# Optimization experiments

Hardware: AMD Instinct MI355X
Metric: run time of the kernel (lower is better)

## Reference

```python
import jax, jax.numpy as jnp
import numpy as np

B, N, D_IN, D_OUT, HH, WW = 64, 512, 256, 32, 160, 160

def setup_inputs() -> dict:
    key = jax.random.key(0)
    k1, k2, k3, k4, k5 = jax.random.split(key, 5)
    return {
        "entity_embeddings": jax.random.normal(k1, (B, N, D_IN), dtype=jnp.float32),
        "weight": jax.random.normal(k2, (D_IN, D_OUT), dtype=jnp.float32) * (1.0 / np.sqrt(D_IN)),
        "bias": jnp.zeros((D_OUT,), dtype=jnp.float32),
        "entity_x": jax.random.randint(k3, (B, N), 0, WW, dtype=jnp.int32),
        "entity_y": jax.random.randint(k4, (B, N), 0, HH, dtype=jnp.int32),
        "entity_num": jax.random.randint(k5, (B,), 1, N, dtype=jnp.int32),
        "H": HH,
        "W": WW,
    }

def reference(entity_embeddings, weight, bias, entity_x, entity_y, entity_num, H, W):
    # fc_block: Linear + ReLU  -> [B, N, D_OUT]
    proj = jax.nn.relu(jnp.einsum('bni,io->bno', entity_embeddings, weight) + bias)
    # mask padded entities (sequence_mask from entity_num)
    mask = (jnp.arange(proj.shape[1])[None, :] < entity_num[:, None]).astype(proj.dtype)
    proj = proj * mask[:, :, None]
    # ScatterConnection ('add'): location = (y, x) -> flat index y*W + x
    flat_idx = entity_y.astype(jnp.int32) * W + entity_x.astype(jnp.int32)  # [B, N]
    b = proj.shape[0]
    out = jnp.zeros((b, H * W, proj.shape[2]), dtype=proj.dtype)
    out = out.at[jnp.arange(b)[:, None], flat_idx].add(proj)  # scatter-add
    # -> [B, D_OUT, H, W]
    scatter_map = out.reshape(b, H, W, proj.shape[2]).transpose(0, 3, 1, 2)
    return scatter_map
```

## Files before the change

kernel.cpp:

```cpp
#include <hip/hip_runtime.h>
#include <stdint.h>

constexpr int DIN  = 256;
constexpr int DOUT = 32;

typedef float f32x4  __attribute__((ext_vector_type(4)));
typedef short bf16x8 __attribute__((ext_vector_type(8)));


__device__ __forceinline__ uint16_t f2bf(float f, float& back) {
    uint32_t u = __builtin_bit_cast(uint32_t, f);
    uint32_t r = (u + 0x7fffu + ((u >> 16) & 1u)) >> 16;
    back = __builtin_bit_cast(float, r << 16);
    return (uint16_t)r;
}

__global__ __launch_bounds__(256)
void k_prep(const float* __restrict__ weight,
            uint16_t* __restrict__ wfh, uint16_t* __restrict__ wfl)
{
    const int id = blockIdx.x * 256 + threadIdx.x;
    const int t    = id >> 7;
    const int h    = (id >> 6) & 1;
    const int lane = id & 63;
    const int kb   = t * 32 + (lane >> 4) * 8;
    const int col  = h * 16 + (lane & 15);
    const int off  = ((t * 2 + h) * 64 + lane) * 8;
    #pragma unroll
    for (int j = 0; j < 8; ++j) {
        float w = weight[(size_t)(kb + j) * DOUT + col];
        float back; uint16_t hi = f2bf(w, back);
        float resid = w - back;
        float b2;  uint16_t lo = f2bf(resid, b2);
        wfh[off + j] = hi;
        wfl[off + j] = lo;
    }
}

__global__ __launch_bounds__(256)
void k_gemm(const float* __restrict__ emb,
            const float* __restrict__ bias,
            const uint16_t* __restrict__ wfh,
            const uint16_t* __restrict__ wfl,
            float* __restrict__ proj,
            int nent)
{
    const int tid  = threadIdx.x;
    const int lane = tid & 63;
    const int wv   = tid >> 6;
    const int eb   = blockIdx.x * 64 + wv * 16;
    const int row  = lane & 15;
    const int kg   = lane >> 4;

    int e = eb + row; if (e >= nent) e = nent - 1;
    const float* erow = emb + (size_t)e * DIN + kg * 8;

    f32x4 acc0 = {0.f, 0.f, 0.f, 0.f};
    f32x4 acc1 = {0.f, 0.f, 0.f, 0.f};

    #pragma unroll
    for (int t = 0; t < 8; ++t) {
        const float4 a0 = *(const float4*)(erow + t * 32);
        const float4 a1 = *(const float4*)(erow + t * 32 + 4);
        const float af[8] = {a0.x, a0.y, a0.z, a0.w, a1.x, a1.y, a1.z, a1.w};
        bf16x8 ahi, alo;
        #pragma unroll
        for (int j = 0; j < 8; ++j) {
            float back; uint16_t h = f2bf(af[j], back);
            float resid = af[j] - back;
            float b2;  uint16_t l = f2bf(resid, b2);
            ahi[j] = (short)h;
            alo[j] = (short)l;
        }
        const int fo = (t * 2) * 64 + lane;
        const bf16x8 bh0 = *(const bf16x8*)&wfh[fo * 8];
        const bf16x8 bh1 = *(const bf16x8*)&wfh[(fo + 64) * 8];
        const bf16x8 bl0 = *(const bf16x8*)&wfl[fo * 8];
        const bf16x8 bl1 = *(const bf16x8*)&wfl[(fo + 64) * 8];
        acc0 = __builtin_amdgcn_mfma_f32_16x16x32_bf16(ahi, bh0, acc0, 0, 0, 0);
        acc1 = __builtin_amdgcn_mfma_f32_16x16x32_bf16(ahi, bh1, acc1, 0, 0, 0);
        acc0 = __builtin_amdgcn_mfma_f32_16x16x32_bf16(alo, bh0, acc0, 0, 0, 0);
        acc1 = __builtin_amdgcn_mfma_f32_16x16x32_bf16(alo, bh1, acc1, 0, 0, 0);
        acc0 = __builtin_amdgcn_mfma_f32_16x16x32_bf16(ahi, bl0, acc0, 0, 0, 0);
        acc1 = __builtin_amdgcn_mfma_f32_16x16x32_bf16(ahi, bl1, acc1, 0, 0, 0);
    }

    const int c0 = lane & 15, c1 = c0 + 16;
    const float b0 = bias[c0], b1 = bias[c1];
    #pragma unroll
    for (int r = 0; r < 4; ++r) {
        const int ent = eb + (lane >> 4) * 4 + r;
        if (ent >= nent) continue;
        proj[(size_t)ent * DOUT + c0] = fmaxf(acc0[r] + b0, 0.f);
        proj[(size_t)ent * DOUT + c1] = fmaxf(acc1[r] + b1, 0.f);
    }
}

__global__ __launch_bounds__(256)
void k_zsplane(const float* __restrict__ proj,
               const int* __restrict__ ex, const int* __restrict__ ey,
               const int* __restrict__ en, const int* __restrict__ pW,
               float* __restrict__ out,
               int N, int nent, int HW)
{
    const int tid = threadIdx.x;
    const int b   = blockIdx.x >> 5;
    const int c   = blockIdx.x & 31;
    float* plane = out + ((size_t)b * DOUT + c) * (size_t)HW;

    if ((HW & 3) == 0) {
        float4* p = (float4*)plane;
        const int n4 = HW >> 2;
        for (int i = tid; i < n4; i += 256)
            p[i] = make_float4(0.f, 0.f, 0.f, 0.f);
    } else {
        for (int i = tid; i < HW; i += 256) plane[i] = 0.f;
    }
    __syncthreads();

    const int cnt = min(en[b], N);
    const int W = *pW;
    const int base = b * N;
    for (int slot = tid; slot < cnt; slot += 256) {
        const int ent = base + slot;
        if (ent >= nent) break;
        const float v = proj[(size_t)ent * DOUT + c];
        if (v != 0.f) {
            const int hw = ey[ent] * W + ex[ent];
            atomicAdd(plane + hw, v);
        }
    }
}

constexpr int FET = 64, FKT = 64, FEP = FKT + 4;
__global__ __launch_bounds__(256)
void enc_fallback(const float* __restrict__ emb, const float* __restrict__ weight,
                  const float* __restrict__ bias, const int* __restrict__ ex,
                  const int* __restrict__ ey, const int* __restrict__ en,
                  const int* __restrict__ pW, float* __restrict__ out,
                  int N, int nent, int HW)
{
    __shared__ float s_emb[FET][FEP];
    __shared__ float s_w[FKT * DOUT];
    const int tid = threadIdx.x;
    const int og = tid & 7, eg = tid >> 3;
    const int eb = blockIdx.x * FET;
    float4 pe[4]; float4 pw[2];
    #pragma unroll
    for (int r = 0; r < 4; ++r) {
        int f = (r << 8) + tid, rw = f >> 4, col = (f & 15) << 2;
        int e = eb + rw; if (e >= nent) e = nent - 1;
        pe[r] = *(const float4*)&emb[(size_t)e * DIN + col];
    }
    #pragma unroll
    for (int r = 0; r < 2; ++r) pw[r] = *(const float4*)&weight[(size_t)(((r << 8) + tid) << 2)];
    float acc[2][4] = {{0,0,0,0},{0,0,0,0}};
    for (int t = 0; t < 4; ++t) {
        #pragma unroll
        for (int r = 0; r < 4; ++r) {
            int f = (r << 8) + tid;
            *(float4*)&s_emb[f >> 4][(f & 15) << 2] = pe[r];
        }
        #pragma unroll
        for (int r = 0; r < 2; ++r) *(float4*)&s_w[((r << 8) + tid) << 2] = pw[r];
        __syncthreads();
        if (t < 3) {
            const int kt = (t + 1) * FKT;
            #pragma unroll
            for (int r = 0; r < 4; ++r) {
                int f = (r << 8) + tid, rw = f >> 4, col = (f & 15) << 2;
                int e = eb + rw; if (e >= nent) e = nent - 1;
                pe[r] = *(const float4*)&emb[(size_t)e * DIN + kt + col];
            }
            #pragma unroll
            for (int r = 0; r < 2; ++r)
                pw[r] = *(const float4*)&weight[(size_t)kt * DOUT + (((r << 8) + tid) << 2)];
        }
        #pragma unroll
        for (int k = 0; k < FKT; k += 4) {
            float4 e0 = *(const float4*)&s_emb[eg][k];
            float4 e1 = *(const float4*)&s_emb[eg + 32][k];
            float4 w0 = *(const float4*)&s_w[(k + 0) * DOUT + og * 4];
            float4 w1 = *(const float4*)&s_w[(k + 1) * DOUT + og * 4];
            float4 w2 = *(const float4*)&s_w[(k + 2) * DOUT + og * 4];
            float4 w3 = *(const float4*)&s_w[(k + 3) * DOUT + og * 4];
            acc[0][0] += e0.x*w0.x + e0.y*w1.x + e0.z*w2.x + e0.w*w3.x;
            acc[0][1] += e0.x*w0.y + e0.y*w1.y + e0.z*w2.y + e0.w*w3.y;
            acc[0][2] += e0.x*w0.z + e0.y*w1.z + e0.z*w2.z + e0.w*w3.z;
            acc[0][3] += e0.x*w0.w + e0.y*w1.w + e0.z*w2.w + e0.w*w3.w;
            acc[1][0] += e1.x*w0.x + e1.y*w1.x + e1.z*w2.x + e1.w*w3.x;
            acc[1][1] += e1.x*w0.y + e1.y*w1.y + e1.z*w2.y + e1.w*w3.y;
            acc[1][2] += e1.x*w0.z + e1.y*w1.z + e1.z*w2.z + e1.w*w3.z;
            acc[1][3] += e1.x*w0.w + e1.y*w1.w + e1.z*w2.w + e1.w*w3.w;
        }
        __syncthreads();
    }
    const int W = *pW;
    const float4 bv = *(const float4*)&bias[og * 4];
    #pragma unroll
    for (int i = 0; i < 2; ++i) {
        int ent = eb + eg + i * 32;
        if (ent >= nent) continue;
        int b = ent / N, n = ent - b * N;
        if (n >= en[b]) continue;
        float* dst = out + ((size_t)b * DOUT + og * 4) * (size_t)HW
                         + (size_t)ey[ent] * W + ex[ent];
        float v0 = fmaxf(acc[i][0] + bv.x, 0.f);
        float v1 = fmaxf(acc[i][1] + bv.y, 0.f);
        float v2 = fmaxf(acc[i][2] + bv.z, 0.f);
        float v3 = fmaxf(acc[i][3] + bv.w, 0.f);
        if (v0 != 0.f) atomicAdd(dst + 0 * (size_t)HW, v0);
        if (v1 != 0.f) atomicAdd(dst + 1 * (size_t)HW, v1);
        if (v2 != 0.f) atomicAdd(dst + 2 * (size_t)HW, v2);
        if (v3 != 0.f) atomicAdd(dst + 3 * (size_t)HW, v3);
    }
}

extern "C" void kernel_launch(void* const* d_in, const int* in_sizes, int n_in,
                              void* d_out, int out_size, void* d_ws, size_t ws_size,
                              hipStream_t stream) {
    const float* emb    = (const float*)d_in[0];
    const float* weight = (const float*)d_in[1];
    const float* bias   = (const float*)d_in[2];
    const int*   ex     = (const int*)d_in[3];
    const int*   ey     = (const int*)d_in[4];
    const int*   en     = (const int*)d_in[5];
    const int*   pW     = (const int*)d_in[7];
    float*       out    = (float*)d_out;

    const int nent = in_sizes[3];
    const int B    = in_sizes[5];
    const int N    = nent / B;
    const int HW   = (int)((size_t)out_size / ((size_t)B * DOUT));

    uint16_t* wfh  = (uint16_t*)d_ws;
    uint16_t* wfl  = (uint16_t*)((char*)d_ws + 16384);
    float*    proj = (float*)((char*)d_ws + 32768);

    const size_t ws_need = 32768 + (size_t)nent * DOUT * sizeof(float);

    if (ws_size >= ws_need) {
        k_prep<<<4, 256, 0, stream>>>(weight, wfh, wfl);
        k_gemm<<<(nent + 63) / 64, 256, 0, stream>>>(emb, bias, wfh, wfl, proj, nent);
        k_zsplane<<<B * DOUT, 256, 0, stream>>>(proj, ex, ey, en, pW, out,
                                                N, nent, HW);
    } else {
        (void)hipMemsetAsync(d_out, 0, (size_t)out_size * sizeof(float), stream);
        const int blocks = (nent + FET - 1) / FET;
        enc_fallback<<<blocks, 256, 0, stream>>>(emb, weight, bias, ex, ey, en, pW,
                                                 out, N, nent, HW);
    }
}
```

Measured before the change: 50.46 us.

## Fuse weight bf16 split into GEMM and split scatter planes across two blocks

Result: faster. 46.47 us, median of 2 (-7.9%).

```diff
diff --git a/kernel.cpp b/kernel.cpp
--- a/kernel.cpp
+++ b/kernel.cpp
@@ -3,10 +3,10 @@
 
 constexpr int DIN  = 256;
 constexpr int DOUT = 32;
+constexpr int ZSPLIT = 2;
 
 typedef float f32x4  __attribute__((ext_vector_type(4)));
 typedef short bf16x8 __attribute__((ext_vector_type(8)));
-
 
 __device__ __forceinline__ uint16_t f2bf(float f, float& back) {
     uint32_t u = __builtin_bit_cast(uint32_t, f);
@@ -16,32 +16,9 @@
 }
 
 __global__ __launch_bounds__(256)
-void k_prep(const float* __restrict__ weight,
-            uint16_t* __restrict__ wfh, uint16_t* __restrict__ wfl)
-{
-    const int id = blockIdx.x * 256 + threadIdx.x;
-    const int t    = id >> 7;
-    const int h    = (id >> 6) & 1;
-    const int lane = id & 63;
-    const int kb   = t * 32 + (lane >> 4) * 8;
-    const int col  = h * 16 + (lane & 15);
-    const int off  = ((t * 2 + h) * 64 + lane) * 8;
-    #pragma unroll
-    for (int j = 0; j < 8; ++j) {
-        float w = weight[(size_t)(kb + j) * DOUT + col];
-        float back; uint16_t hi = f2bf(w, back);
-        float resid = w - back;
-        float b2;  uint16_t lo = f2bf(resid, b2);
-        wfh[off + j] = hi;
-        wfl[off + j] = lo;
-    }
-}
-
-__global__ __launch_bounds__(256)
 void k_gemm(const float* __restrict__ emb,
+            const float* __restrict__ weight,
             const float* __restrict__ bias,
-            const uint16_t* __restrict__ wfh,
-            const uint16_t* __restrict__ wfl,
             float* __restrict__ proj,
             int nent)
 {
@@ -62,21 +39,36 @@
     for (int t = 0; t < 8; ++t) {
         const float4 a0 = *(const float4*)(erow + t * 32);
         const float4 a1 = *(const float4*)(erow + t * 32 + 4);
+        const float* wp = weight + (size_t)(t * 32 + kg * 8) * DOUT + row;
+        float wf0[8], wf1[8];
+        #pragma unroll
+        for (int j = 0; j < 8; ++j) {
+            wf0[j] = wp[(size_t)j * DOUT];
+            wf1[j] = wp[(size_t)j * DOUT + 16];
+        }
         const float af[8] = {a0.x, a0.y, a0.z, a0.w, a1.x, a1.y, a1.z, a1.w};
-        bf16x8 ahi, alo;
-        #pragma unroll
-        for (int j = 0; j < 8; ++j) {
-            float back; uint16_t h = f2bf(af[j], back);
-            float resid = af[j] - back;
-            float b2;  uint16_t l = f2bf(resid, b2);
-            ahi[j] = (short)h;
-            alo[j] = (short)l;
-        }
-        const int fo = (t * 2) * 64 + lane;
-        const bf16x8 bh0 = *(const bf16x8*)&wfh[fo * 8];
-        const bf16x8 bh1 = *(const bf16x8*)&wfh[(fo + 64) * 8];
-        const bf16x8 bl0 = *(const bf16x8*)&wfl[fo * 8];
-        const bf16x8 bl1 = *(const bf16x8*)&wfl[(fo + 64) * 8];
+        bf16x8 ahi, alo, bh0, bl0, bh1, bl1;
+        #pragma unroll
+        for (int j = 0; j < 8; ++j) {
+            float back, b2;
+            const uint16_t h = f2bf(af[j], back);
+            const uint16_t l = f2bf(af[j] - back, b2);
+            ahi[j] = (short)h; alo[j] = (short)l;
+        }
+        #pragma unroll
+        for (int j = 0; j < 8; ++j) {
+            float back, b2;
+            const uint16_t h = f2bf(wf0[j], back);
+            const uint16_t l = f2bf(wf0[j] - back, b2);
+            bh0[j] = (short)h; bl0[j] = (short)l;
+        }
+        #pragma unroll
+        for (int j = 0; j < 8; ++j) {
+            float back, b2;
+            const uint16_t h = f2bf(wf1[j], back);
+            const uint16_t l = f2bf(wf1[j] - back, b2);
+            bh1[j] = (short)h; bl1[j] = (short)l;
+        }
         acc0 = __builtin_amdgcn_mfma_f32_16x16x32_bf16(ahi, bh0, acc0, 0, 0, 0);
         acc1 = __builtin_amdgcn_mfma_f32_16x16x32_bf16(ahi, bh1, acc1, 0, 0, 0);
         acc0 = __builtin_amdgcn_mfma_f32_16x16x32_bf16(alo, bh0, acc0, 0, 0, 0);
@@ -97,38 +89,39 @@
 }
 
 __global__ __launch_bounds__(256)
-void k_zsplane(const float* __restrict__ proj,
-               const int* __restrict__ ex, const int* __restrict__ ey,
-               const int* __restrict__ en, const int* __restrict__ pW,
-               float* __restrict__ out,
-               int N, int nent, int HW)
+void k_zs(const float* __restrict__ proj,
+          const int* __restrict__ ex, const int* __restrict__ ey,
+          const int* __restrict__ en, const int* __restrict__ pW,
+          float* __restrict__ out,
+          int N, int nent, int HW)
 {
     const int tid = threadIdx.x;
-    const int b   = blockIdx.x >> 5;
-    const int c   = blockIdx.x & 31;
+    const int idx = blockIdx.x;
+    const int h   = idx & (ZSPLIT - 1);
+    const int c   = (idx >> 1) & 31;
+    const int b   = idx >> 6;
+
     float* plane = out + ((size_t)b * DOUT + c) * (size_t)HW;
-
-    if ((HW & 3) == 0) {
-        float4* p = (float4*)plane;
-        const int n4 = HW >> 2;
-        for (int i = tid; i < n4; i += 256)
-            p[i] = make_float4(0.f, 0.f, 0.f, 0.f);
-    } else {
-        for (int i = tid; i < HW; i += 256) plane[i] = 0.f;
-    }
+    const int seglen = HW / ZSPLIT;
+    const int s0 = h * seglen;
+
+    float4* p = (float4*)(plane + s0);
+    const int n4 = seglen >> 2;
+    for (int i = tid; i < n4; i += 256)
+        p[i] = make_float4(0.f, 0.f, 0.f, 0.f);
     __syncthreads();
 
     const int cnt = min(en[b], N);
     const int W = *pW;
     const int base = b * N;
+    const int send = s0 + seglen;
     for (int slot = tid; slot < cnt; slot += 256) {
         const int ent = base + slot;
         if (ent >= nent) break;
+        const int hw = ey[ent] * W + ex[ent];
+        if (hw < s0 || hw >= send) continue;
         const float v = proj[(size_t)ent * DOUT + c];
-        if (v != 0.f) {
-            const int hw = ey[ent] * W + ex[ent];
-            atomicAdd(plane + hw, v);
-        }
+        if (v != 0.f) atomicAdd(plane + hw, v);
     }
 }
 
@@ -231,19 +224,20 @@
     const int nent = in_sizes[3];
     const int B    = in_sizes[5];
     const int N    = nent / B;
+    const int DIN_rt = in_sizes[0] / nent;
     const int HW   = (int)((size_t)out_size / ((size_t)B * DOUT));
 
-    uint16_t* wfh  = (uint16_t*)d_ws;
-    uint16_t* wfl  = (uint16_t*)((char*)d_ws + 16384);
-    float*    proj = (float*)((char*)d_ws + 32768);
-
-    const size_t ws_need = 32768 + (size_t)nent * DOUT * sizeof(float);
-
-    if (ws_size >= ws_need) {
-        k_prep<<<4, 256, 0, stream>>>(weight, wfh, wfl);
-        k_gemm<<<(nent + 63) / 64, 256, 0, stream>>>(emb, bias, wfh, wfl, proj, nent);
-        k_zsplane<<<B * DOUT, 256, 0, stream>>>(proj, ex, ey, en, pW, out,
-                                                N, nent, HW);
+    float* proj = (float*)d_ws;
+    const size_t ws_need = (size_t)nent * DOUT * sizeof(float);
+
+    const bool fused_ok = (ws_size >= ws_need) && (DIN_rt == DIN) &&
+                          (in_sizes[2] == DOUT) && (B * N == nent) &&
+                          (HW % (4 * ZSPLIT) == 0);
+
+    if (fused_ok) {
+        k_gemm<<<(nent + 63) / 64, 256, 0, stream>>>(emb, weight, bias, proj, nent);
+        k_zs<<<B * DOUT * ZSPLIT, 256, 0, stream>>>(proj, ex, ey, en, pW, out,
+                                                    N, nent, HW);
     } else {
         (void)hipMemsetAsync(d_out, 0, (size_t)out_size * sizeof(float), stream);
         const int blocks = (nent + FET - 1) / FET;
```
